# Optimization experiments

Measured on AMD Instinct MI355X. Metric: run time of the kernel, lower is better.

## Reference

```python
import jax, jax.numpy as jnp
import numpy as np

N, D, S, M = 32, 128, 128, 64
BASIS = 5


def setup_inputs() -> dict:
    key = jax.random.key(0)
    k1, k2 = jax.random.split(key)
    inputs = jax.random.normal(k1, (N, D, M, M), dtype=jnp.float32)
    coeffs = jax.random.normal(k2, (D, S, BASIS), dtype=jnp.float32) * np.sqrt(2.0) / (D + S)
    all_bias = jnp.zeros((1, S, 1, 1), dtype=jnp.float32)
    return {"inputs": inputs, "coeffs": coeffs, "all_bias": all_bias}


def reference(inputs, coeffs, all_bias):
    # inputs: [N, D, m, m]
    m = inputs.shape[3]
    diag_part = jnp.diagonal(inputs, axis1=2, axis2=3)          # [N, D, m]
    mean_diag = jnp.mean(diag_part, axis=2, keepdims=True)      # [N, D, 1]
    mean_cols = jnp.mean(inputs, axis=2)                        # [N, D, m]
    mean_all = jnp.mean(mean_cols, axis=2)                      # [N, D]

    op1 = (mean_cols[:, :, :, None] + mean_cols[:, :, None, :]) / 2   # [N, D, m, m]
    op2 = inputs
    op3 = (diag_part[:, :, :, None] + diag_part[:, :, None, :]) / 2
    op4 = jnp.broadcast_to(mean_diag[:, :, :, None], inputs.shape)
    op5 = jnp.broadcast_to(mean_all[:, :, None, None], inputs.shape)

    ops_out = jnp.stack([op1, op2, op3, op4, op5], axis=2)      # [N, D, 5, m, m]
    output = jnp.einsum('dsb,ndbij->nsij', coeffs, ops_out)     # [N, S, m, m]
    return output + all_bias
```

## Files before the change

### kernel.cpp

```cpp
#include <hip/hip_runtime.h>

#define NN 32
#define DD 128
#define SS 128
#define MM 64
#define PP 4096
#define DSZ (DD * SS)

typedef short bf16x8 __attribute__((ext_vector_type(8)));
typedef float f32x4  __attribute__((ext_vector_type(4)));

#define OFF_CPK 0
#define OFF_C1T (OFF_CPK + 5 * DSZ)
#define OFF_MC  (OFF_C1T + DSZ / 2)
#define OFF_DG  (OFF_MC + NN * DD * MM)
#define OFF_MD  (OFF_DG + NN * DD * MM)
#define OFF_MA  (OFF_MD + NN * DD)
#define OFF_UP  (OFF_MA + NN * DD)

__device__ __forceinline__ unsigned int fbits(float f) {
    union { float f; unsigned int u; } c; c.f = f; return c.u;
}

__global__ __launch_bounds__(256) void pack_k(const float* __restrict__ coeffs,
                                              float* __restrict__ cpk,
                                              unsigned short* __restrict__ c1t) {
    int g = blockIdx.x * 256 + threadIdx.x;
    int d = g >> 7, s = g & 127;
    float v0 = coeffs[g * 5 + 0];
    float v1 = coeffs[g * 5 + 1];
    float v2 = coeffs[g * 5 + 2];
    float v3 = coeffs[g * 5 + 3];
    float v4 = coeffs[g * 5 + 4];
    cpk[0 * DSZ + g] = v0;
    cpk[2 * DSZ + g] = v2;
    cpk[3 * DSZ + g] = v3;
    cpk[4 * DSZ + g] = v4;
    unsigned int u = fbits(v1);
    u += 0x7fffu + ((u >> 16) & 1);
    c1t[s * DD + d] = (unsigned short)(u >> 16);
}

__global__ __launch_bounds__(256) void stats_k(const float* __restrict__ x,
                                               float* __restrict__ mc,
                                               float* __restrict__ dg,
                                               float* __restrict__ md,
                                               float* __restrict__ ma) {
    int nd = blockIdx.x * 4 + (threadIdx.x >> 6);
    int l  = threadIdx.x & 63;
    const float* base = x + (size_t)nd * PP;
    int iq = l >> 4, jq = l & 15;

    float4 cs = make_float4(0.f, 0.f, 0.f, 0.f);
    float dv = 0.f;
#pragma unroll
    for (int r = 0; r < 16; ++r) {
        float4 v = *(const float4*)(base + (r * 4 + iq) * MM + jq * 4);
        cs.x += v.x; cs.y += v.y; cs.z += v.z; cs.w += v.w;
        if (r == jq)
            dv = (iq == 0) ? v.x : (iq == 1) ? v.y : (iq == 2) ? v.z : v.w;
    }
#pragma unroll
    for (int m = 16; m <= 32; m <<= 1) {
        cs.x += __shfl_xor(cs.x, m);
        cs.y += __shfl_xor(cs.y, m);
        cs.z += __shfl_xor(cs.z, m);
        cs.w += __shfl_xor(cs.w, m);
    }
    if (iq == 0) {
        float4 o = make_float4(cs.x * (1.f / 64.f), cs.y * (1.f / 64.f),
                               cs.z * (1.f / 64.f), cs.w * (1.f / 64.f));
        *(float4*)(mc + nd * MM + jq * 4) = o;
    }
    dg[nd * MM + 4 * jq + iq] = dv;
    float dsum = dv;
#pragma unroll
    for (int m = 1; m <= 32; m <<= 1) dsum += __shfl_xor(dsum, m);
    float tot = cs.x + cs.y + cs.z + cs.w;
#pragma unroll
    for (int m = 1; m <= 8; m <<= 1) tot += __shfl_xor(tot, m);
    if (l == 0) {
        md[nd] = dsum * (1.f / 64.f);
        ma[nd] = tot * (1.f / 4096.f);
    }
}

__global__ __launch_bounds__(256) void combine_k(const float* __restrict__ cpk,
                                                 const float* __restrict__ mc,
                                                 const float* __restrict__ dg,
                                                 const float* __restrict__ md,
                                                 const float* __restrict__ ma,
                                                 const float* __restrict__ bias,
                                                 float* __restrict__ up) {
    int sg = blockIdx.x, n = blockIdx.y;
    int t  = threadIdx.x;
    int i  = t & 63;
    int sq = t >> 6;
    int s0 = sg * 16 + sq * 4;

    const float* c0p = cpk + 0 * DSZ;
    const float* c2p = cpk + 2 * DSZ;
    const float* c3p = cpk + 3 * DSZ;
    const float* c4p = cpk + 4 * DSZ;

    float wacc[4] = {0.f, 0.f, 0.f, 0.f};
    float vacc[4] = {0.f, 0.f, 0.f, 0.f};
#pragma unroll 2
    for (int d = 0; d < DD; ++d) {
        int bidx = (n * DD + d) * MM + i;
        float m  = mc[bidx];
        float g  = dg[bidx];
        float mdv = md[n * DD + d];
        float mav = ma[n * DD + d];
#pragma unroll
        for (int r = 0; r < 4; ++r) {
            int cs = d * SS + s0 + r;
            wacc[r] += c0p[cs] * m + c2p[cs] * g;
            vacc[r] += c3p[cs] * mdv + c4p[cs] * mav;
        }
    }
#pragma unroll
    for (int r = 0; r < 4; ++r) {
        int s = s0 + r;
        up[((size_t)n * SS + s) * MM + i] = 0.5f * (wacc[r] + vacc[r] + bias[s]);
    }
}

#define USTR 68
__global__ __launch_bounds__(256, 3) void gemm_k(const float* __restrict__ x,
                                                 const unsigned short* __restrict__ c1t,
                                                 const float* __restrict__ up,
                                                 float* __restrict__ out) {
    __shared__ float us[SS * USTR];

    int n  = blockIdx.y;
    int p0 = blockIdx.x * 128;
    int t  = threadIdx.x;
    int w  = t >> 6, l = t & 63;
    int wp = w & 1, wsn = w >> 1;
    int q  = l >> 4, c = l & 15;

    const float* upn = up + (size_t)n * SS * MM;
#pragma unroll
    for (int e = t; e < SS * MM / 4; e += 256) {
        int s  = e >> 4;
        int i4 = (e & 15) * 4;
        *(f32x4*)&us[s * USTR + i4] = *(const f32x4*)(upn + s * MM + i4);
    }
    __syncthreads();

    int p0w = p0 + wp * 64;
    int s0w = wsn * 64;
    int iw  = p0w >> 6;
    const float* xb = x + (size_t)n * DD * PP;

    f32x4 acc[4][4];
#pragma unroll
    for (int a = 0; a < 4; ++a)
#pragma unroll
        for (int b = 0; b < 4; ++b) acc[a][b] = (f32x4)0.f;

#pragma unroll
    for (int kt = 0; kt < 4; ++kt) {
        int k0 = kt * 32 + q * 8;
        bf16x8 af[4];
#pragma unroll
        for (int st = 0; st < 4; ++st)
            af[st] = *(const bf16x8*)(c1t + (size_t)(s0w + st * 16 + c) * DD + k0);
#pragma unroll
        for (int pt = 0; pt < 4; ++pt) {
            const float* xp = xb + (size_t)k0 * PP + (p0w + pt * 16 + c);
            float f0 = xp[0 * PP], f1 = xp[1 * PP], f2 = xp[2 * PP], f3 = xp[3 * PP];
            float f4 = xp[4 * PP], f5 = xp[5 * PP], f6 = xp[6 * PP], f7 = xp[7 * PP];
            union { unsigned int u[4]; bf16x8 v; } bb;
            bb.u[0] = __builtin_amdgcn_perm(fbits(f1), fbits(f0), 0x07060302u);
            bb.u[1] = __builtin_amdgcn_perm(fbits(f3), fbits(f2), 0x07060302u);
            bb.u[2] = __builtin_amdgcn_perm(fbits(f5), fbits(f4), 0x07060302u);
            bb.u[3] = __builtin_amdgcn_perm(fbits(f7), fbits(f6), 0x07060302u);
#pragma unroll
            for (int st = 0; st < 4; ++st)
                acc[st][pt] = __builtin_amdgcn_mfma_f32_16x16x32_bf16(af[st], bb.v,
                                                                     acc[st][pt], 0, 0, 0);
        }
    }

#pragma unroll
    for (int st = 0; st < 4; ++st) {
#pragma unroll
        for (int r = 0; r < 4; ++r) {
            int s = s0w + st * 16 + q * 4 + r;
            float uiv = us[s * USTR + iw];
            float* orow = out + ((size_t)(n * SS + s)) * PP;
#pragma unroll
            for (int pt = 0; pt < 4; ++pt) {
                int p = p0w + pt * 16 + c;
                int j = p & 63;
                orow[p] = acc[st][pt][r] + uiv + us[s * USTR + j];
            }
        }
    }
}

extern "C" void kernel_launch(void* const* d_in, const int* in_sizes, int n_in,
                              void* d_out, int out_size, void* d_ws, size_t ws_size,
                              hipStream_t stream) {
    const float* x      = (const float*)d_in[0];
    const float* coeffs = (const float*)d_in[1];
    const float* bias   = (const float*)d_in[2];
    float* out = (float*)d_out;
    float* ws  = (float*)d_ws;

    float*          cpk = ws + OFF_CPK;
    unsigned short* c1t = (unsigned short*)(ws + OFF_C1T);
    float*          mc  = ws + OFF_MC;
    float*          dg  = ws + OFF_DG;
    float*          md  = ws + OFF_MD;
    float*          ma  = ws + OFF_MA;
    float*          up  = ws + OFF_UP;

    pack_k<<<DSZ / 256, 256, 0, stream>>>(coeffs, cpk, c1t);
    stats_k<<<NN * DD / 4, 256, 0, stream>>>(x, mc, dg, md, ma);
    combine_k<<<dim3(8, NN), 256, 0, stream>>>(cpk, mc, dg, md, ma, bias, up);
    gemm_k<<<dim3(PP / 128, NN), 256, 0, stream>>>(x, c1t, up, out);
}
```

Before: 171.2 us.

## Fold coefficient packing into stats kernel, retile GEMM warps, use nontemporal stores

Removes the separate pack kernel. The bf16 transpose of the op2 coefficients now runs inside the first 64 blocks of the stats kernel, and the combine kernel reads the strided raw coeffs directly instead of repacked planes. The GEMM warp tiling changes from 64x64 per wave (2x2 waves) to all 128 output channels by 32 positions per wave, so every wave loads all A fragments and fewer x columns. Output stores become nontemporal to avoid polluting the cache. This saves one launch and a workspace round trip, but it raises register pressure in the GEMM and makes the coefficient reads in combine strided.

Result: slower. 179.3 us (+4.7%).

```diff
diff --git a/kernel.cpp b/kernel.cpp
--- a/kernel.cpp
+++ b/kernel.cpp
@@ -10,8 +10,7 @@
 typedef short bf16x8 __attribute__((ext_vector_type(8)));
 typedef float f32x4  __attribute__((ext_vector_type(4)));
 
-#define OFF_CPK 0
-#define OFF_C1T (OFF_CPK + 5 * DSZ)
+#define OFF_C1T 0
 #define OFF_MC  (OFF_C1T + DSZ / 2)
 #define OFF_DG  (OFF_MC + NN * DD * MM)
 #define OFF_MD  (OFF_DG + NN * DD * MM)
@@ -22,30 +21,21 @@
     union { float f; unsigned int u; } c; c.f = f; return c.u;
 }
 
-__global__ __launch_bounds__(256) void pack_k(const float* __restrict__ coeffs,
-                                              float* __restrict__ cpk,
-                                              unsigned short* __restrict__ c1t) {
-    int g = blockIdx.x * 256 + threadIdx.x;
-    int d = g >> 7, s = g & 127;
-    float v0 = coeffs[g * 5 + 0];
-    float v1 = coeffs[g * 5 + 1];
-    float v2 = coeffs[g * 5 + 2];
-    float v3 = coeffs[g * 5 + 3];
-    float v4 = coeffs[g * 5 + 4];
-    cpk[0 * DSZ + g] = v0;
-    cpk[2 * DSZ + g] = v2;
-    cpk[3 * DSZ + g] = v3;
-    cpk[4 * DSZ + g] = v4;
-    unsigned int u = fbits(v1);
-    u += 0x7fffu + ((u >> 16) & 1);
-    c1t[s * DD + d] = (unsigned short)(u >> 16);
-}
-
 __global__ __launch_bounds__(256) void stats_k(const float* __restrict__ x,
+                                               const float* __restrict__ coeffs,
                                                float* __restrict__ mc,
                                                float* __restrict__ dg,
                                                float* __restrict__ md,
-                                               float* __restrict__ ma) {
+                                               float* __restrict__ ma,
+                                               unsigned short* __restrict__ c1t) {
+    if (blockIdx.x < 64) {
+        int g = blockIdx.x * 256 + threadIdx.x;
+        float v = coeffs[(((g & 127) << 7) + (g >> 7)) * 5 + 1];
+        unsigned int u = fbits(v);
+        u += 0x7fffu + ((u >> 16) & 1);
+        c1t[g] = (unsigned short)(u >> 16);
+    }
+
     int nd = blockIdx.x * 4 + (threadIdx.x >> 6);
     int l  = threadIdx.x & 63;
     const float* base = x + (size_t)nd * PP;
@@ -85,7 +75,7 @@
     }
 }
 
-__global__ __launch_bounds__(256) void combine_k(const float* __restrict__ cpk,
+__global__ __launch_bounds__(256) void combine_k(const float* __restrict__ coeffs,
                                                  const float* __restrict__ mc,
                                                  const float* __restrict__ dg,
                                                  const float* __restrict__ md,
@@ -98,25 +88,20 @@
     int sq = t >> 6;
     int s0 = sg * 16 + sq * 4;
 
-    const float* c0p = cpk + 0 * DSZ;
-    const float* c2p = cpk + 2 * DSZ;
-    const float* c3p = cpk + 3 * DSZ;
-    const float* c4p = cpk + 4 * DSZ;
-
     float wacc[4] = {0.f, 0.f, 0.f, 0.f};
     float vacc[4] = {0.f, 0.f, 0.f, 0.f};
 #pragma unroll 2
     for (int d = 0; d < DD; ++d) {
         int bidx = (n * DD + d) * MM + i;
-        float m  = mc[bidx];
-        float g  = dg[bidx];
+        float m   = mc[bidx];
+        float g   = dg[bidx];
         float mdv = md[n * DD + d];
         float mav = ma[n * DD + d];
 #pragma unroll
         for (int r = 0; r < 4; ++r) {
-            int cs = d * SS + s0 + r;
-            wacc[r] += c0p[cs] * m + c2p[cs] * g;
-            vacc[r] += c3p[cs] * mdv + c4p[cs] * mav;
+            const float* cp = coeffs + (size_t)(d * SS + s0 + r) * 5;
+            wacc[r] += cp[0] * m + cp[2] * g;
+            vacc[r] += cp[3] * mdv + cp[4] * mav;
         }
     }
 #pragma unroll
@@ -137,7 +122,6 @@
     int p0 = blockIdx.x * 128;
     int t  = threadIdx.x;
     int w  = t >> 6, l = t & 63;
-    int wp = w & 1, wsn = w >> 1;
     int q  = l >> 4, c = l & 15;
 
     const float* upn = up + (size_t)n * SS * MM;
@@ -149,26 +133,25 @@
     }
     __syncthreads();
 
-    int p0w = p0 + wp * 64;
-    int s0w = wsn * 64;
+    int p0w = p0 + w * 32;
     int iw  = p0w >> 6;
     const float* xb = x + (size_t)n * DD * PP;
 
-    f32x4 acc[4][4];
-#pragma unroll
-    for (int a = 0; a < 4; ++a)
-#pragma unroll
-        for (int b = 0; b < 4; ++b) acc[a][b] = (f32x4)0.f;
+    f32x4 acc[8][2];
+#pragma unroll
+    for (int a = 0; a < 8; ++a)
+#pragma unroll
+        for (int b = 0; b < 2; ++b) acc[a][b] = (f32x4)0.f;
 
 #pragma unroll
     for (int kt = 0; kt < 4; ++kt) {
         int k0 = kt * 32 + q * 8;
-        bf16x8 af[4];
-#pragma unroll
-        for (int st = 0; st < 4; ++st)
-            af[st] = *(const bf16x8*)(c1t + (size_t)(s0w + st * 16 + c) * DD + k0);
-#pragma unroll
-        for (int pt = 0; pt < 4; ++pt) {
+        bf16x8 af[8];
+#pragma unroll
+        for (int st = 0; st < 8; ++st)
+            af[st] = *(const bf16x8*)(c1t + (size_t)(st * 16 + c) * DD + k0);
+#pragma unroll
+        for (int pt = 0; pt < 2; ++pt) {
             const float* xp = xb + (size_t)k0 * PP + (p0w + pt * 16 + c);
             float f0 = xp[0 * PP], f1 = xp[1 * PP], f2 = xp[2 * PP], f3 = xp[3 * PP];
             float f4 = xp[4 * PP], f5 = xp[5 * PP], f6 = xp[6 * PP], f7 = xp[7 * PP];
@@ -178,24 +161,24 @@
             bb.u[2] = __builtin_amdgcn_perm(fbits(f5), fbits(f4), 0x07060302u);
             bb.u[3] = __builtin_amdgcn_perm(fbits(f7), fbits(f6), 0x07060302u);
 #pragma unroll
-            for (int st = 0; st < 4; ++st)
+            for (int st = 0; st < 8; ++st)
                 acc[st][pt] = __builtin_amdgcn_mfma_f32_16x16x32_bf16(af[st], bb.v,
                                                                      acc[st][pt], 0, 0, 0);
         }
     }
 
 #pragma unroll
-    for (int st = 0; st < 4; ++st) {
+    for (int st = 0; st < 8; ++st) {
 #pragma unroll
         for (int r = 0; r < 4; ++r) {
-            int s = s0w + st * 16 + q * 4 + r;
+            int s = st * 16 + q * 4 + r;
             float uiv = us[s * USTR + iw];
             float* orow = out + ((size_t)(n * SS + s)) * PP;
 #pragma unroll
-            for (int pt = 0; pt < 4; ++pt) {
+            for (int pt = 0; pt < 2; ++pt) {
                 int p = p0w + pt * 16 + c;
-                int j = p & 63;
-                orow[p] = acc[st][pt][r] + uiv + us[s * USTR + j];
+                __builtin_nontemporal_store(acc[st][pt][r] + uiv + us[s * USTR + (p & 63)],
+                                            orow + p);
             }
         }
     }
@@ -210,7 +193,6 @@
     float* out = (float*)d_out;
     float* ws  = (float*)d_ws;
 
-    float*          cpk = ws + OFF_CPK;
     unsigned short* c1t = (unsigned short*)(ws + OFF_C1T);
     float*          mc  = ws + OFF_MC;
     float*          dg  = ws + OFF_DG;
@@ -218,8 +200,7 @@
     float*          ma  = ws + OFF_MA;
     float*          up  = ws + OFF_UP;
 
-    pack_k<<<DSZ / 256, 256, 0, stream>>>(coeffs, cpk, c1t);
-    stats_k<<<NN * DD / 4, 256, 0, stream>>>(x, mc, dg, md, ma);
-    combine_k<<<dim3(8, NN), 256, 0, stream>>>(cpk, mc, dg, md, ma, bias, up);
+    stats_k<<<NN * DD / 4, 256, 0, stream>>>(x, coeffs, mc, dg, md, ma, c1t);
+    combine_k<<<dim3(8, NN), 256, 0, stream>>>(coeffs, mc, dg, md, ma, bias, up);
     gemm_k<<<dim3(PP / 128, NN), 256, 0, stream>>>(x, c1t, up, out);
 }
```
